# Performance work log

Measured on AMD Instinct MI355X. Metric: run time of the kernel, lower is better.

Reference implementation:

```python
import jax, jax.numpy as jnp
import numpy as np
import math

RCR = 5.2
NUM_SPECIES = 7
AEV_DIM = 1008
WIDTHS = [1008, 256, 192, 160]


def setup_inputs() -> dict:
    key = jax.random.key(0)
    ks = jax.random.split(key, 12)
    B, N = 1, 2048
    species = jax.random.randint(ks[0], (B, N), 0, NUM_SPECIES, dtype=jnp.int64 if jax.config.read('jax_enable_x64') else jnp.int32)
    coordinates = jax.random.uniform(ks[1], (B, N, 3), dtype=jnp.float32) * 6.0
    EtaR = jnp.array([16.0], dtype=jnp.float32)
    ShfR = jnp.array([0.9 + 0.18 * x for x in range(16)], dtype=jnp.float32)
    s = 0.05
    W0 = jax.random.normal(ks[2], (NUM_SPECIES, WIDTHS[1], WIDTHS[0]), jnp.float32) * s
    b0 = jax.random.normal(ks[3], (NUM_SPECIES, WIDTHS[1]), jnp.float32) * s
    W1 = jax.random.normal(ks[4], (NUM_SPECIES, WIDTHS[2], WIDTHS[1]), jnp.float32) * s
    b1 = jax.random.normal(ks[5], (NUM_SPECIES, WIDTHS[2]), jnp.float32) * s
    W2 = jax.random.normal(ks[6], (NUM_SPECIES, WIDTHS[3], WIDTHS[2]), jnp.float32) * s
    b2 = jax.random.normal(ks[7], (NUM_SPECIES, WIDTHS[3]), jnp.float32) * s
    Wf = jax.random.normal(ks[8], (NUM_SPECIES, 1, WIDTHS[3]), jnp.float32) * s
    bf = jax.random.normal(ks[9], (NUM_SPECIES, 1), jnp.float32) * s
    return {'species': species, 'coordinates': coordinates, 'EtaR': EtaR, 'ShfR': ShfR,
            'W0': W0, 'b0': b0, 'W1': W1, 'b1': b1, 'W2': W2, 'b2': b2, 'Wf': Wf, 'bf': bf}


def _celu(x, alpha=0.1):
    return jnp.maximum(x, 0.0) + jnp.minimum(0.0, alpha * jnp.expm1(x / alpha))


def _aev(species, coordinates, EtaR, ShfR):
    B, N = species.shape
    diff = coordinates[:, :, None, :] - coordinates[:, None, :, :]  # [B,N,N,3]
    dsq = jnp.sum(diff * diff, axis=-1)
    safe = jnp.where(dsq > 0, dsq, 1.0)
    dist = jnp.sqrt(safe)  # [B,N,N], diag is a dummy 1.0
    mask = (dsq > 0) & (dist <= RCR)
    fc = (0.5 * jnp.cos(math.pi * dist / RCR) + 0.5) * mask.astype(jnp.float32)
    onehot = jax.nn.one_hot(species, NUM_SPECIES, dtype=jnp.float32)  # [B,N,S]
    core = jnp.exp(-EtaR[0] * (dist[..., None] - ShfR) ** 2)  # [B,N,N,R]
    weighted = core * fc[..., None]
    # sum over neighbor j, grouped by neighbor species s (species-major concat order)
    radial = jnp.einsum('bijr,bjs->bisr', weighted, onehot)  # [B,N,S,R]
    radial = radial.reshape(B, N, NUM_SPECIES * ShfR.shape[0])
    pad = AEV_DIM - radial.shape[-1]
    return jnp.pad(radial, ((0, 0), (0, 0), (0, pad)))


def reference(species, coordinates, EtaR, ShfR, W0, b0, W1, b1, W2, b2, Wf, bf):
    aev = _aev(species, coordinates, EtaR, ShfR)  # [B,N,1008]
    # run all 7 element nets on every atom (matches the module's redundant-compute semantics)
    h = _celu(jnp.einsum('soh,bnh->sbno', W0, aev) + b0[:, None, None, :])
    h = _celu(jnp.einsum('soh,sbnh->sbno', W1, h) + b1[:, None, None, :])
    h = _celu(jnp.einsum('soh,sbnh->sbno', W2, h) + b2[:, None, None, :])
    e = jnp.einsum('soh,sbnh->sbno', Wf, h) + bf[:, None, None, :]  # [S,B,N,1]
    onehot = jax.nn.one_hot(species, NUM_SPECIES, dtype=jnp.float32)  # [B,N,S]
    total = jnp.einsum('sbn,bns->', e[..., 0], onehot)
    return total.reshape(1)
```

## Files before the change

### kernel.cpp

```cpp
#include <hip/hip_runtime.h>

#define N_ATOMS 2048
#define NSPEC 7
#define NR 16
#define NFEAT 112
#define K0P 128
#define RCR_F 5.2f
#define H0 256
#define H1 192
#define H2 160
#define W0_PITCH 1008
#define MT 16
#define NTILE16 (N_ATOMS / MT)

typedef __attribute__((ext_vector_type(8))) short short8;
typedef __attribute__((ext_vector_type(4))) float floatx4;

#define WS_SEG     0
#define WS_SCOORD  16384
#define WS_AEVB    65536
#define WS_WB0     2621440
#define WS_WB1     3145728
#define WS_WB2     3866624

#define S0E (NSPEC * H0 * K0P)
#define S1E (NSPEC * H1 * H0)
#define S2E (NSPEC * H2 * H1)
#define PREP_TOT (S0E + S1E + S2E)

__device__ __forceinline__ float celu01(float x) {
    return x > 0.f ? x : 0.1f * (__expf(x * 10.f) - 1.f);
}

__device__ __forceinline__ unsigned short f2bf(float x) {
    unsigned int u = __float_as_uint(x);
    u = (u + 0x7FFFu + ((u >> 16) & 1u)) >> 16;
    return (unsigned short)u;
}

__global__ __launch_bounds__(256) void setup_kernel(const int* __restrict__ species,
                                                    const float* __restrict__ coords,
                                                    const float* __restrict__ W0,
                                                    const float* __restrict__ W1,
                                                    const float* __restrict__ W2,
                                                    int* __restrict__ seg,
                                                    float4* __restrict__ scoord,
                                                    unsigned short* __restrict__ wb0,
                                                    unsigned short* __restrict__ wb1,
                                                    unsigned short* __restrict__ wb2,
                                                    float* __restrict__ out) {
    int t = threadIdx.x;
    if (blockIdx.x == 0) {
        __shared__ int cnt[NSPEC];
        __shared__ int cur[NSPEC];
        if (t < NSPEC) cnt[t] = 0;
        __syncthreads();
        for (int a = t; a < N_ATOMS; a += 256) atomicAdd(&cnt[species[a]], 1);
        __syncthreads();
        if (t == 0) {
            int run = 0;
            for (int s = 0; s < NSPEC; s++) { seg[s] = run; cur[s] = run; run += cnt[s]; }
            seg[NSPEC] = run;
            out[0] = 0.0f;
        }
        __syncthreads();
        for (int a = t; a < N_ATOMS; a += 256) {
            int sp = species[a];
            int pos = atomicAdd(&cur[sp], 1);
            scoord[pos] = make_float4(coords[3*a], coords[3*a+1], coords[3*a+2], 0.f);
        }
    } else {
        int idx = (blockIdx.x - 1) * 256 + t;
        if (idx < S0E) {
            int k = idx & 127, r = idx >> 7;
            float v = (k < NFEAT) ? W0[(size_t)r * W0_PITCH + k] : 0.f;
            wb0[idx] = f2bf(v);
        } else if (idx < S0E + S1E) {
            wb1[idx - S0E] = f2bf(W1[idx - S0E]);
        } else {
            wb2[idx - S0E - S1E] = f2bf(W2[idx - S0E - S1E]);
        }
    }
}

__global__ __launch_bounds__(256) void aev_kernel(const float4* __restrict__ scoord,
                                                  const int* __restrict__ seg,
                                                  const float* __restrict__ ShfR,
                                                  const float* __restrict__ EtaR,
                                                  unsigned short* __restrict__ aevb) {
    int s = blockIdx.y;
    int p = blockIdx.x * 4 + (threadIdx.x >> 6);
    int lane = threadIdx.x & 63;

    float4 ci = scoord[p];
    float eta = EtaR[0];
    float shf[NR];
#pragma unroll
    for (int r = 0; r < NR; r++) shf[r] = ShfR[r];
    float acc[NR];
#pragma unroll
    for (int r = 0; r < NR; r++) acc[r] = 0.f;

    int kbeg = seg[s] + lane;
    int kend = seg[s + 1];
    const float rc2 = RCR_F * RCR_F;
    const float cosk = 3.14159265358979f / RCR_F;

    for (int k = kbeg; k < kend; k += 64) {
        float4 cj = scoord[k];
        float dx = ci.x - cj.x, dy = ci.y - cj.y, dz = ci.z - cj.z;
        float dsq = dx*dx + dy*dy + dz*dz;
        bool valid = (dsq > 0.f) && (dsq <= rc2);
        float d = sqrtf(dsq);
        float fc = 0.5f * __cosf(d * cosk) + 0.5f;
        fc = valid ? fc : 0.f;
#pragma unroll
        for (int r = 0; r < NR; r++) {
            float u = d - shf[r];
            acc[r] = fmaf(__expf(-eta * u * u), fc, acc[r]);
        }
    }
#pragma unroll
    for (int r = 0; r < NR; r++) {
        float v = acc[r];
        v += __shfl_xor(v, 1);
        v += __shfl_xor(v, 2);
        v += __shfl_xor(v, 4);
        v += __shfl_xor(v, 8);
        v += __shfl_xor(v, 16);
        v += __shfl_xor(v, 32);
        acc[r] = v;
    }
    if (lane == 0) {
        unsigned short* dst = aevb + (size_t)p * K0P + s * NR;
#pragma unroll
        for (int r = 0; r < NR; r++) dst[r] = f2bf(acc[r]);
        if (s == 0) {
            unsigned short* pz = aevb + (size_t)p * K0P + NFEAT;
#pragma unroll
            for (int r = 0; r < K0P - NFEAT; r++) pz[r] = 0;
        }
    }
}

__global__ __launch_bounds__(256) void mlp_fused(const unsigned short* __restrict__ aevb,
                                                 const unsigned short* __restrict__ wb0,
                                                 const unsigned short* __restrict__ wb1,
                                                 const unsigned short* __restrict__ wb2,
                                                 const float* __restrict__ b0,
                                                 const float* __restrict__ b1,
                                                 const float* __restrict__ b2,
                                                 const float* __restrict__ Wf,
                                                 const float* __restrict__ bf,
                                                 const int* __restrict__ seg,
                                                 float* __restrict__ out) {
    __shared__ unsigned short aevs[MT][K0P + 8];
    __shared__ unsigned short h0s[MT][H0 + 8];
    __shared__ unsigned short h1s[MT][H1 + 8];

    int s = blockIdx.y;
    int segend = seg[s + 1];
    int base = seg[s] + blockIdx.x * MT;
    if (base >= segend) return;
    int n_act = min(MT, segend - base);

    int t = threadIdx.x;
    int w = t >> 6, lane = t & 63;
    int r = lane & 15, quad = lane >> 4;

    {
        int row = t >> 4, chunk = t & 15;
        const short8* src = (const short8*)(aevb + (size_t)(base + row) * K0P + chunk * 8);
        *(short8*)&aevs[row][chunk * 8] = *src;
    }
    __syncthreads();

#pragma unroll
    for (int it = 0; it < 4; it++) {
        int nbase = (it * 4 + w) * 16;
        const unsigned short* brow = wb0 + ((size_t)(s * H0 + nbase + r)) * K0P + quad * 8;
        floatx4 acc = {0.f, 0.f, 0.f, 0.f};
#pragma unroll
        for (int ks = 0; ks < K0P / 32; ks++) {
            short8 a = *(const short8*)&aevs[r][ks * 32 + quad * 8];
            short8 b = *(const short8*)(brow + ks * 32);
            acc = __builtin_amdgcn_mfma_f32_16x16x32_bf16(a, b, acc, 0, 0, 0);
        }
        float bi = b0[s * H0 + nbase + r];
#pragma unroll
        for (int reg = 0; reg < 4; reg++)
            h0s[quad * 4 + reg][nbase + r] = f2bf(celu01(acc[reg] + bi));
    }
    __syncthreads();

#pragma unroll
    for (int it = 0; it < 3; it++) {
        int nbase = (it * 4 + w) * 16;
        const unsigned short* brow = wb1 + ((size_t)(s * H1 + nbase + r)) * H0 + quad * 8;
        floatx4 acc = {0.f, 0.f, 0.f, 0.f};
#pragma unroll
        for (int ks = 0; ks < H0 / 32; ks++) {
            short8 a = *(const short8*)&h0s[r][ks * 32 + quad * 8];
            short8 b = *(const short8*)(brow + ks * 32);
            acc = __builtin_amdgcn_mfma_f32_16x16x32_bf16(a, b, acc, 0, 0, 0);
        }
        float bi = b1[s * H1 + nbase + r];
#pragma unroll
        for (int reg = 0; reg < 4; reg++)
            h1s[quad * 4 + reg][nbase + r] = f2bf(celu01(acc[reg] + bi));
    }
    __syncthreads();

    float e = 0.f;
#pragma unroll
    for (int it = 0; it < 3; it++) {
        int nt = it * 4 + w;
        if (nt >= H2 / 16) break;
        int nbase = nt * 16;
        const unsigned short* brow = wb2 + ((size_t)(s * H2 + nbase + r)) * H1 + quad * 8;
        floatx4 acc = {0.f, 0.f, 0.f, 0.f};
#pragma unroll
        for (int ks = 0; ks < H1 / 32; ks++) {
            short8 a = *(const short8*)&h1s[r][ks * 32 + quad * 8];
            short8 b = *(const short8*)(brow + ks * 32);
            acc = __builtin_amdgcn_mfma_f32_16x16x32_bf16(a, b, acc, 0, 0, 0);
        }
        float bi = b2[s * H2 + nbase + r];
        float wf = Wf[s * H2 + nbase + r];
#pragma unroll
        for (int reg = 0; reg < 4; reg++) {
            int atom = base + quad * 4 + reg;
            if (atom < segend) e += wf * celu01(acc[reg] + bi);
        }
    }
    if (t == 0) e += (float)n_act * bf[s];

    e += __shfl_xor(e, 1);
    e += __shfl_xor(e, 2);
    e += __shfl_xor(e, 4);
    e += __shfl_xor(e, 8);
    e += __shfl_xor(e, 16);
    e += __shfl_xor(e, 32);
    if (lane == 0) atomicAdd(out, e);
}

extern "C" void kernel_launch(void* const* d_in, const int* in_sizes, int n_in,
                              void* d_out, int out_size, void* d_ws, size_t ws_size,
                              hipStream_t stream) {
    const int*   species = (const int*)d_in[0];
    const float* coords  = (const float*)d_in[1];
    const float* EtaR    = (const float*)d_in[2];
    const float* ShfR    = (const float*)d_in[3];
    const float* W0      = (const float*)d_in[4];
    const float* b0      = (const float*)d_in[5];
    const float* W1      = (const float*)d_in[6];
    const float* b1      = (const float*)d_in[7];
    const float* W2      = (const float*)d_in[8];
    const float* b2      = (const float*)d_in[9];
    const float* Wf      = (const float*)d_in[10];
    const float* bf      = (const float*)d_in[11];
    float* out = (float*)d_out;
    char* ws = (char*)d_ws;

    int*            seg    = (int*)(ws + WS_SEG);
    float4*         scoord = (float4*)(ws + WS_SCOORD);
    unsigned short* aevb   = (unsigned short*)(ws + WS_AEVB);
    unsigned short* wb0    = (unsigned short*)(ws + WS_WB0);
    unsigned short* wb1    = (unsigned short*)(ws + WS_WB1);
    unsigned short* wb2    = (unsigned short*)(ws + WS_WB2);

    hipLaunchKernelGGL(setup_kernel, dim3(1 + PREP_TOT / 256), dim3(256), 0, stream,
                       species, coords, W0, W1, W2, seg, scoord, wb0, wb1, wb2, out);
    hipLaunchKernelGGL(aev_kernel, dim3(N_ATOMS / 4, NSPEC), dim3(256), 0, stream,
                       scoord, seg, ShfR, EtaR, aevb);
    hipLaunchKernelGGL(mlp_fused, dim3(NTILE16, NSPEC), dim3(256), 0, stream,
                       aevb, wb0, wb1, wb2, b0, b1, b2, Wf, bf, seg, out);
}
```

Before: 134.4 us.

## Use raw exp/cos intrinsics, transpose-reduce AEV sums, and widen MLP blocks to 512 threads

```diff
diff --git a/kernel.cpp b/kernel.cpp
--- a/kernel.cpp
+++ b/kernel.cpp
@@ -94,6 +94,7 @@
 
     float4 ci = scoord[p];
     float eta = EtaR[0];
+    const float ceta = -eta * 1.44269504089f;
     float shf[NR];
 #pragma unroll
     for (int r = 0; r < NR; r++) shf[r] = ShfR[r];
@@ -104,46 +105,56 @@
     int kbeg = seg[s] + lane;
     int kend = seg[s + 1];
     const float rc2 = RCR_F * RCR_F;
-    const float cosk = 3.14159265358979f / RCR_F;
+    const float cosk = 0.5f / RCR_F;
 
     for (int k = kbeg; k < kend; k += 64) {
         float4 cj = scoord[k];
         float dx = ci.x - cj.x, dy = ci.y - cj.y, dz = ci.z - cj.z;
-        float dsq = dx*dx + dy*dy + dz*dz;
+        float dsq = fmaf(dx, dx, fmaf(dy, dy, dz * dz));
         bool valid = (dsq > 0.f) && (dsq <= rc2);
         float d = sqrtf(dsq);
-        float fc = 0.5f * __cosf(d * cosk) + 0.5f;
-        fc = valid ? fc : 0.f;
+        float cr;
+        asm("v_cos_f32 %0, %1" : "=v"(cr) : "v"(d * cosk));
+        float fc = valid ? fmaf(0.5f, cr, 0.5f) : 0.f;
 #pragma unroll
         for (int r = 0; r < NR; r++) {
             float u = d - shf[r];
-            acc[r] = fmaf(__expf(-eta * u * u), fc, acc[r]);
-        }
-    }
-#pragma unroll
-    for (int r = 0; r < NR; r++) {
-        float v = acc[r];
-        v += __shfl_xor(v, 1);
-        v += __shfl_xor(v, 2);
-        v += __shfl_xor(v, 4);
-        v += __shfl_xor(v, 8);
-        v += __shfl_xor(v, 16);
-        v += __shfl_xor(v, 32);
-        acc[r] = v;
-    }
-    if (lane == 0) {
-        unsigned short* dst = aevb + (size_t)p * K0P + s * NR;
-#pragma unroll
-        for (int r = 0; r < NR; r++) dst[r] = f2bf(acc[r]);
-        if (s == 0) {
-            unsigned short* pz = aevb + (size_t)p * K0P + NFEAT;
-#pragma unroll
-            for (int r = 0; r < K0P - NFEAT; r++) pz[r] = 0;
-        }
-    }
-}
-
-__global__ __launch_bounds__(256) void mlp_fused(const unsigned short* __restrict__ aevb,
+            float a = ceta * (u * u);
+            float e;
+            asm("v_exp_f32 %0, %1" : "=v"(e) : "v"(a));
+            acc[r] = fmaf(e, fc, acc[r]);
+        }
+    }
+
+#define MERGE_ROUND(D, NV)                                            \
+    {                                                                 \
+        bool hi = (lane & (D)) != 0;                                  \
+        _Pragma("unroll")                                             \
+        for (int i = 0; i < (NV) / 2; i++) {                          \
+            float a = acc[2 * i], b = acc[2 * i + 1];                 \
+            float send = hi ? a : b;                                  \
+            float keep = hi ? b : a;                                  \
+            acc[i] = keep + __shfl_xor(send, (D));                    \
+        }                                                             \
+    }
+    MERGE_ROUND(1, 16)
+    MERGE_ROUND(2, 8)
+    MERGE_ROUND(4, 4)
+    MERGE_ROUND(8, 2)
+#undef MERGE_ROUND
+    float v = acc[0];
+    v += __shfl_xor(v, 16);
+    v += __shfl_xor(v, 32);
+
+    unsigned short* dst = aevb + (size_t)p * K0P + s * NR;
+    if (lane < NR) {
+        dst[lane] = f2bf(v);
+    } else if (s == 0 && lane < NR + (K0P - NFEAT)) {
+        aevb[(size_t)p * K0P + NFEAT + (lane - NR)] = 0;
+    }
+}
+
+__global__ __launch_bounds__(512) void mlp_fused(const unsigned short* __restrict__ aevb,
                                                  const unsigned short* __restrict__ wb0,
                                                  const unsigned short* __restrict__ wb1,
                                                  const unsigned short* __restrict__ wb2,
@@ -168,7 +179,7 @@
     int w = t >> 6, lane = t & 63;
     int r = lane & 15, quad = lane >> 4;
 
-    {
+    if (t < 256) {
         int row = t >> 4, chunk = t & 15;
         const short8* src = (const short8*)(aevb + (size_t)(base + row) * K0P + chunk * 8);
         *(short8*)&aevs[row][chunk * 8] = *src;
@@ -176,8 +187,8 @@
     __syncthreads();
 
 #pragma unroll
-    for (int it = 0; it < 4; it++) {
-        int nbase = (it * 4 + w) * 16;
+    for (int it = 0; it < 2; it++) {
+        int nbase = (it * 8 + w) * 16;
         const unsigned short* brow = wb0 + ((size_t)(s * H0 + nbase + r)) * K0P + quad * 8;
         floatx4 acc = {0.f, 0.f, 0.f, 0.f};
 #pragma unroll
@@ -194,43 +205,47 @@
     __syncthreads();
 
 #pragma unroll
-    for (int it = 0; it < 3; it++) {
-        int nbase = (it * 4 + w) * 16;
-        const unsigned short* brow = wb1 + ((size_t)(s * H1 + nbase + r)) * H0 + quad * 8;
-        floatx4 acc = {0.f, 0.f, 0.f, 0.f};
-#pragma unroll
-        for (int ks = 0; ks < H0 / 32; ks++) {
-            short8 a = *(const short8*)&h0s[r][ks * 32 + quad * 8];
-            short8 b = *(const short8*)(brow + ks * 32);
-            acc = __builtin_amdgcn_mfma_f32_16x16x32_bf16(a, b, acc, 0, 0, 0);
-        }
-        float bi = b1[s * H1 + nbase + r];
-#pragma unroll
-        for (int reg = 0; reg < 4; reg++)
-            h1s[quad * 4 + reg][nbase + r] = f2bf(celu01(acc[reg] + bi));
+    for (int it = 0; it < 2; it++) {
+        int nt = it * 8 + w;
+        if (nt < H1 / 16) {
+            int nbase = nt * 16;
+            const unsigned short* brow = wb1 + ((size_t)(s * H1 + nbase + r)) * H0 + quad * 8;
+            floatx4 acc = {0.f, 0.f, 0.f, 0.f};
+#pragma unroll
+            for (int ks = 0; ks < H0 / 32; ks++) {
+                short8 a = *(const short8*)&h0s[r][ks * 32 + quad * 8];
+                short8 b = *(const short8*)(brow + ks * 32);
+                acc = __builtin_amdgcn_mfma_f32_16x16x32_bf16(a, b, acc, 0, 0, 0);
+            }
+            float bi = b1[s * H1 + nbase + r];
+#pragma unroll
+            for (int reg = 0; reg < 4; reg++)
+                h1s[quad * 4 + reg][nbase + r] = f2bf(celu01(acc[reg] + bi));
+        }
     }
     __syncthreads();
 
     float e = 0.f;
 #pragma unroll
-    for (int it = 0; it < 3; it++) {
-        int nt = it * 4 + w;
-        if (nt >= H2 / 16) break;
-        int nbase = nt * 16;
-        const unsigned short* brow = wb2 + ((size_t)(s * H2 + nbase + r)) * H1 + quad * 8;
-        floatx4 acc = {0.f, 0.f, 0.f, 0.f};
-#pragma unroll
-        for (int ks = 0; ks < H1 / 32; ks++) {
-            short8 a = *(const short8*)&h1s[r][ks * 32 + quad * 8];
-            short8 b = *(const short8*)(brow + ks * 32);
-            acc = __builtin_amdgcn_mfma_f32_16x16x32_bf16(a, b, acc, 0, 0, 0);
-        }
-        float bi = b2[s * H2 + nbase + r];
-        float wf = Wf[s * H2 + nbase + r];
-#pragma unroll
-        for (int reg = 0; reg < 4; reg++) {
-            int atom = base + quad * 4 + reg;
-            if (atom < segend) e += wf * celu01(acc[reg] + bi);
+    for (int it = 0; it < 2; it++) {
+        int nt = it * 8 + w;
+        if (nt < H2 / 16) {
+            int nbase = nt * 16;
+            const unsigned short* brow = wb2 + ((size_t)(s * H2 + nbase + r)) * H1 + quad * 8;
+            floatx4 acc = {0.f, 0.f, 0.f, 0.f};
+#pragma unroll
+            for (int ks = 0; ks < H1 / 32; ks++) {
+                short8 a = *(const short8*)&h1s[r][ks * 32 + quad * 8];
+                short8 b = *(const short8*)(brow + ks * 32);
+                acc = __builtin_amdgcn_mfma_f32_16x16x32_bf16(a, b, acc, 0, 0, 0);
+            }
+            float bi = b2[s * H2 + nbase + r];
+            float wf = Wf[s * H2 + nbase + r];
+#pragma unroll
+            for (int reg = 0; reg < 4; reg++) {
+                int atom = base + quad * 4 + reg;
+                if (atom < segend) e += wf * celu01(acc[reg] + bi);
+            }
         }
     }
     if (t == 0) e += (float)n_act * bf[s];
@@ -273,6 +288,6 @@
                        species, coords, W0, W1, W2, seg, scoord, wb0, wb1, wb2, out);
     hipLaunchKernelGGL(aev_kernel, dim3(N_ATOMS / 4, NSPEC), dim3(256), 0, stream,
                        scoord, seg, ShfR, EtaR, aevb);
-    hipLaunchKernelGGL(mlp_fused, dim3(NTILE16, NSPEC), dim3(256), 0, stream,
+    hipLaunchKernelGGL(mlp_fused, dim3(NTILE16, NSPEC), dim3(512), 0, stream,
                        aevb, wb0, wb1, wb2, b0, b1, b2, Wf, bf, seg, out);
 }
```

Measured after the change: 133.1 us, median of 2. Within noise of the previous version (-1.0%).
